# Kernel optimization log

Hardware: AMD Instinct MI355X
Metric: run time of the kernel (lower is better)

## Reference

```python
import jax, jax.numpy as jnp
import numpy as np

C = 256
NH = 4  # attention heads
G = 8   # groupnorm groups
EPS = 1e-5


def group_norm(x, weight, bias):
    B, Cc, H, W = x.shape
    xg = x.reshape(B, G, Cc // G, H, W)
    mean = xg.mean(axis=(2, 3, 4), keepdims=True)
    var = xg.var(axis=(2, 3, 4), keepdims=True)
    xg = (xg - mean) * jax.lax.rsqrt(var + EPS)
    xn = xg.reshape(B, Cc, H, W)
    return xn * weight[None, :, None, None] + bias[None, :, None, None]


def setup_inputs() -> dict:
    key = jax.random.key(0)
    ks = jax.random.split(key, 7)
    B, H, W = 16, 32, 32
    x = jax.random.normal(ks[0], (B, C, H, W), dtype=jnp.float32)
    n_weight = jnp.ones((C,), dtype=jnp.float32)
    n_bias = jnp.zeros((C,), dtype=jnp.float32)
    qkv_w = jax.random.normal(ks[1], (3 * C, C), dtype=jnp.float32) * (C ** -0.5)
    qkv_b = jnp.zeros((3 * C,), dtype=jnp.float32)
    p_w = jax.random.normal(ks[2], (C, C), dtype=jnp.float32) * (C ** -0.5)
    p_b = jnp.zeros((C,), dtype=jnp.float32)
    return {"x": x, "n_weight": n_weight, "n_bias": n_bias,
            "qkv_w": qkv_w, "qkv_b": qkv_b, "p_w": p_w, "p_b": p_b}


def reference(x, n_weight, n_bias, qkv_w, qkv_b, p_w, p_b):
    B, Cc, H, W = x.shape
    N = H * W
    dh = Cc // NH
    sc = dh ** -0.5
    xn = group_norm(x, n_weight, n_bias)  # [B,C,H,W]
    xn_flat = xn.reshape(B, Cc, N)
    # 1x1 conv == channel matmul
    qkv = jnp.einsum('oc,bcn->bon', qkv_w, xn_flat) + qkv_b[None, :, None]
    qkv = qkv.reshape(B, 3, NH, dh, N)
    q, k, v = qkv[:, 0], qkv[:, 1], qkv[:, 2]  # [B,h,dh,N]
    a = jax.nn.softmax(jnp.einsum('bhci,bhcj->bhij', q, k) * sc, axis=-1)
    o = jnp.einsum('bhij,bhcj->bhci', a, v).reshape(B, Cc, N)
    proj = jnp.einsum('oc,bcn->bon', p_w, o) + p_b[None, :, None]
    return x + proj.reshape(B, Cc, H, W)
```

## Files before the change

kernel.cpp:

```cpp
#include <hip/hip_runtime.h>
#include <math.h>

typedef unsigned short ushort;
typedef unsigned int uint;
typedef __attribute__((ext_vector_type(8))) short bf16x8;
typedef __attribute__((ext_vector_type(4))) float f32x4;
typedef __attribute__((ext_vector_type(16))) float f32x16;
typedef __attribute__((ext_vector_type(2))) unsigned uint2v;

constexpr int Bc  = 16;
constexpr float EPSc = 1e-5f;
constexpr float QSC  = 0.18033688f;

__device__ inline ushort f2bf(float f) {
    uint u = __float_as_uint(f);
    uint r = (u + 0x7fffu + ((u >> 16) & 1u)) >> 16;
    return (ushort)r;
}
__device__ __forceinline__ uint cvt2(float a, float b) {
    uint r;
    asm("v_cvt_pk_bf16_f32 %0, %1, %2" : "=v"(r) : "v"(a), "v"(b));
    return r;
}
__device__ __forceinline__ ushort f2bf_fast(float f) {
    uint r;
    asm("v_cvt_pk_bf16_f32 %0, %1, %2" : "=v"(r) : "v"(f), "v"(f));
    return (ushort)r;
}
__device__ __forceinline__ uint2v plswap(uint a, uint b) {
#if __has_builtin(__builtin_amdgcn_permlane32_swap)
    return __builtin_amdgcn_permlane32_swap(a, b, false, false);
#else
    asm volatile("v_permlane32_swap_b32 %0, %1" : "+v"(a), "+v"(b));
    uint2v r; r.x = a; r.y = b; return r;
#endif
}
#if __has_builtin(__builtin_amdgcn_exp2f)
#define EXP2F(x) __builtin_amdgcn_exp2f(x)
#else
#define EXP2F(x) __expf((x) * 0.69314718f)
#endif
__device__ __forceinline__ void gl_lds16(const ushort* g, ushort* l) {
    __builtin_amdgcn_global_load_lds(
        (const __attribute__((address_space(1))) void*)g,
        (__attribute__((address_space(3))) void*)l, 16, 0, 0);
}

__global__ __launch_bounds__(1024, 4) void norm_k(
    const float* __restrict__ x, const float* __restrict__ nw,
    const float* __restrict__ nb, const float* __restrict__ qkvw,
    const float* __restrict__ pw, ushort* __restrict__ xt,
    ushort* __restrict__ wqb, ushort* __restrict__ pwb) {
    int blk = blockIdx.x;
    int t = threadIdx.x;
    if (blk < 128) {
        int b = blk >> 3, g = blk & 7;
        const float* xs = x + ((size_t)(b * 8 + g)) * 32768;
        const float4* p4 = (const float4*)xs;
        float s = 0.f, s2 = 0.f;
#pragma unroll
        for (int i = 0; i < 8; ++i) {
            float4 v = p4[t + i * 1024];
            s += (v.x + v.y) + (v.z + v.w);
            s2 += (v.x * v.x + v.y * v.y) + (v.z * v.z + v.w * v.w);
        }
#pragma unroll
        for (int off = 1; off < 64; off <<= 1) {
            s += __shfl_xor(s, off);
            s2 += __shfl_xor(s2, off);
        }
        __shared__ float rs[16], rq[16], bc[2];
        int wv = t >> 6, lane = t & 63;
        if (lane == 0) { rs[wv] = s; rq[wv] = s2; }
        __syncthreads();
        if (t == 0) {
            float ts = 0.f, tq = 0.f;
#pragma unroll
            for (int i = 0; i < 16; ++i) { ts += rs[i]; tq += rq[i]; }
            float mean = ts * (1.f / 32768.f);
            float var  = tq * (1.f / 32768.f) - mean * mean;
            bc[0] = mean; bc[1] = rsqrtf(var + EPSc);
        }
        __syncthreads();
        float mean = bc[0], inv = bc[1];
        int n = t;
        uint w[16];
#pragma unroll
        for (int c = 0; c < 32; c += 2) {
            float w0 = inv * nw[g * 32 + c];
            float b0 = nb[g * 32 + c] - mean * w0;
            float w1 = inv * nw[g * 32 + c + 1];
            float b1 = nb[g * 32 + c + 1] - mean * w1;
            float v0 = xs[(size_t)c * 1024 + n] * w0 + b0;
            float v1 = xs[(size_t)(c + 1) * 1024 + n] * w1 + b1;
            w[c >> 1] = cvt2(v0, v1);
        }
        ushort* dst = &xt[((size_t)(b * 1024 + n)) * 256 + g * 32];
#pragma unroll
        for (int i = 0; i < 4; ++i) {
            uint4 u; u.x = w[i*4]; u.y = w[i*4+1]; u.z = w[i*4+2]; u.w = w[i*4+3];
            *(uint4*)&dst[i * 8] = u;
        }
    } else {
        int idx = ((blk - 128) * 1024 + t) * 4;
        if (idx < 196608) {
            int row = idx >> 8;
            float sc = (row < 256) ? QSC : 1.f;
            float4 v = *(const float4*)&qkvw[idx];
            uint2 u; u.x = cvt2(v.x * sc, v.y * sc); u.y = cvt2(v.z * sc, v.w * sc);
            *(uint2*)&wqb[idx] = u;
        } else {
            int j = idx - 196608;
            float4 v = *(const float4*)&pw[j];
            uint2 u; u.x = cvt2(v.x, v.y); u.y = cvt2(v.z, v.w);
            *(uint2*)&pwb[j] = u;
        }
    }
}

__global__ __launch_bounds__(256, 2) void qkv_gemm_k(
    const ushort* __restrict__ wq, const ushort* __restrict__ xt,
    const float* __restrict__ wb, ushort* __restrict__ qkT,
    ushort* __restrict__ vbuf) {
    int b = blockIdx.z, cy = blockIdx.y, sx = blockIdx.x;
    __shared__ ushort SB[2][2][128 * 64];
    int t = threadIdx.x, lane = t & 63, w = t >> 6;
    int quad = lane >> 4, l15 = lane & 15;
    int wm = w >> 1, wn = w & 1;
    const ushort* wrow = wq + (size_t)cy * 128 * 256;
    const ushort* xrow = xt + ((size_t)b * 1024 + sx * 128) * 256;
    bool tpath = (cy < 4);
    int r0 = t >> 3;
    int cs = (t & 7) ^ (r0 & 7);
    int dst = t * 8;
#pragma unroll
    for (int ps = 0; ps < 4; ++ps) {
        int r = r0 + ps * 32;
        gl_lds16(&wrow[(size_t)r * 256 + cs * 8], &SB[0][0][ps * 2048 + dst]);
        gl_lds16(&xrow[(size_t)r * 256 + cs * 8], &SB[0][1][ps * 2048 + dst]);
    }
    __syncthreads();
    int s0 = quad ^ (l15 & 7);
    f32x4 acc[4][4] = {};
    int cur = 0;
    for (int ki = 0; ki < 4; ++ki) {
        if (ki < 3) {
            int k0 = (ki + 1) * 64, nx = cur ^ 1;
#pragma unroll
            for (int ps = 0; ps < 4; ++ps) {
                int r = r0 + ps * 32;
                gl_lds16(&wrow[(size_t)r * 256 + k0 + cs * 8], &SB[nx][0][ps * 2048 + dst]);
                gl_lds16(&xrow[(size_t)r * 256 + k0 + cs * 8], &SB[nx][1][ps * 2048 + dst]);
            }
        }
        const ushort* Wc = SB[cur][0];
        const ushort* Xc = SB[cur][1];
        const ushort* Am = tpath ? Xc : Wc;
        const ushort* Bn = tpath ? Wc : Xc;
#pragma unroll
        for (int kk = 0; kk < 2; ++kk) {
            int sl = s0 ^ (kk * 4);
            bf16x8 fa[4], fb[4];
#pragma unroll
            for (int mi = 0; mi < 4; ++mi)
                fa[mi] = *(const bf16x8*)&Am[(wm * 64 + mi * 16 + l15) * 64 + sl * 8];
#pragma unroll
            for (int ni = 0; ni < 4; ++ni)
                fb[ni] = *(const bf16x8*)&Bn[(wn * 64 + ni * 16 + l15) * 64 + sl * 8];
#pragma unroll
            for (int mi = 0; mi < 4; ++mi)
#pragma unroll
                for (int ni = 0; ni < 4; ++ni)
                    acc[mi][ni] = __builtin_amdgcn_mfma_f32_16x16x32_bf16(
                        fa[mi], fb[ni], acc[mi][ni], 0, 0, 0);
        }
        __syncthreads();
        cur ^= 1;
    }
    __syncthreads();
    ushort* Tw = ((ushort*)SB) + w * (64 * 72);
    float bsc = (tpath && cy < 2) ? QSC : 1.f;
    if (tpath) {
#pragma unroll
        for (int ni = 0; ni < 4; ++ni) {
            float bias = wb[cy * 128 + wn * 64 + ni * 16 + l15] * bsc;
#pragma unroll
            for (int mi = 0; mi < 4; ++mi)
#pragma unroll
                for (int rr = 0; rr < 4; ++rr)
                    Tw[(mi * 16 + quad * 4 + rr) * 72 + ni * 16 + l15] =
                        f2bf_fast(acc[mi][ni][rr] + bias);
        }
    } else {
#pragma unroll
        for (int mi = 0; mi < 4; ++mi)
#pragma unroll
            for (int rr = 0; rr < 4; ++rr) {
                float bias = wb[cy * 128 + wm * 64 + mi * 16 + quad * 4 + rr];
#pragma unroll
                for (int ni = 0; ni < 4; ++ni)
                    Tw[(mi * 16 + quad * 4 + rr) * 72 + ni * 16 + l15] =
                        f2bf_fast(acc[mi][ni][rr] + bias);
            }
    }
    __asm__ __volatile__("" ::: "memory");
    int row8 = lane >> 3, ch = lane & 7;
#pragma unroll
    for (int p = 0; p < 8; ++p) {
        int row = p * 8 + row8;
        uint4 u = *(const uint4*)&Tw[row * 72 + ch * 8];
        if (tpath) {
            int sp = sx * 128 + wm * 64 + row;
            *(uint4*)&qkT[((size_t)b * 1024 + sp) * 512 + cy * 128 + wn * 64 + ch * 8] = u;
        } else {
            int chanloc = (cy - 4) * 128 + wm * 64 + row;
            *(uint4*)&vbuf[((size_t)b * 256 + chanloc) * 1024 + sx * 128 + wn * 64 + ch * 8] = u;
        }
    }
}

__global__ __launch_bounds__(256, 2) void attn_k(
    const ushort* __restrict__ qkT, const ushort* __restrict__ vbuf,
    ushort* __restrict__ ot) {
    int bh = blockIdx.x;
    int i0 = blockIdx.y * 128;
    int b = bh >> 2, h = bh & 3;
    const ushort* qTb = qkT + (size_t)b * 1024 * 512 + h * 64;
    const ushort* kTb = qTb + 256;
    const ushort* vb  = vbuf + ((size_t)(b * 256 + h * 64)) * 1024;
    __shared__ ushort SM[16384];
    ushort* Ks0 = SM;
    ushort* Vs0 = SM + 8192;
    int t = threadIdx.x, lane = t & 63, wv = t >> 6;
    int l31 = lane & 31, hf = lane >> 5;
    int r0 = t >> 3, pc = t & 7;
#pragma unroll
    for (int seg = 0; seg < 2; ++seg) {
        int row = seg * 32 + r0;
        int c = pc ^ (row & 7);
        gl_lds16(&kTb[(size_t)row * 512 + c * 8], &Ks0[seg * 2048 + t * 8]);
        gl_lds16(&vb[(size_t)row * 1024 + c * 8], &Vs0[seg * 2048 + t * 8]);
    }
    bf16x8 qf[4];
#pragma unroll
    for (int ks = 0; ks < 4; ++ks)
        qf[ks] = *(const bf16x8*)
            &qTb[(size_t)(i0 + wv * 32 + l31) * 512 + ks * 16 + hf * 8];
    __syncthreads();
    f32x16 oT0 = {}, oT1 = {};
    float lsum = 0.f;
    int cur = 0;
    for (int j0 = 0; j0 < 1024; j0 += 64) {
        ushort* Kc = Ks0 + cur * 4096;
        ushort* Vc = Vs0 + cur * 4096;
        if (j0 < 960) {
            int nx = cur ^ 1;
            ushort* Kn = Ks0 + nx * 4096;
            ushort* Vn = Vs0 + nx * 4096;
#pragma unroll
            for (int seg = 0; seg < 2; ++seg) {
                int row = seg * 32 + r0;
                int c = pc ^ (row & 7);
                gl_lds16(&kTb[(size_t)(j0 + 64 + row) * 512 + c * 8], &Kn[seg * 2048 + t * 8]);
                gl_lds16(&vb[(size_t)row * 1024 + j0 + 64 + c * 8],   &Vn[seg * 2048 + t * 8]);
            }
        }
#pragma unroll
        for (int jb = 0; jb < 2; ++jb) {
            f32x16 s = {};
            __builtin_amdgcn_s_setprio(1);
#pragma unroll
            for (int ks = 0; ks < 4; ++ks) {
                int row = jb * 32 + l31;
                int c = (2 * ks + hf) ^ (row & 7);
                bf16x8 ak = *(const bf16x8*)&Kc[row * 64 + c * 8];
                s = __builtin_amdgcn_mfma_f32_32x32x16_bf16(ak, qf[ks], s, 0, 0, 0);
            }
            __builtin_amdgcn_s_setprio(0);
            float e[16];
#pragma unroll
            for (int r = 0; r < 16; ++r) e[r] = EXP2F(s[r]);
            lsum += ((e[0] + e[1]) + (e[2] + e[3])) + ((e[4] + e[5]) + (e[6] + e[7]))
                  + ((e[8] + e[9]) + (e[10] + e[11])) + ((e[12] + e[13]) + (e[14] + e[15]));
            uint w0[4], w1[4];
#pragma unroll
            for (int q = 0; q < 4; ++q) {
                w0[q] = cvt2(e[q * 4 + 0], e[q * 4 + 1]);
                w1[q] = cvt2(e[q * 4 + 2], e[q * 4 + 3]);
            }
            bf16x8 pf[2];
#pragma unroll
            for (int s2 = 0; s2 < 2; ++s2) {
                uint2v ra = plswap(w0[2 * s2], w0[2 * s2 + 1]);
                uint2v rb = plswap(w1[2 * s2], w1[2 * s2 + 1]);
                uint4 u; u.x = ra.x; u.y = rb.x; u.z = ra.y; u.w = rb.y;
                bf16x8 v; __builtin_memcpy(&v, &u, 16);
                pf[s2] = v;
            }
            __builtin_amdgcn_s_setprio(1);
#pragma unroll
            for (int s2 = 0; s2 < 2; ++s2) {
#pragma unroll
                for (int db = 0; db < 2; ++db) {
                    int row = db * 32 + l31;
                    int c = (2 * (jb * 2 + s2) + hf) ^ (row & 7);
                    bf16x8 av = *(const bf16x8*)&Vc[row * 64 + c * 8];
                    if (db == 0)
                        oT0 = __builtin_amdgcn_mfma_f32_32x32x16_bf16(av, pf[s2], oT0, 0, 0, 0);
                    else
                        oT1 = __builtin_amdgcn_mfma_f32_32x32x16_bf16(av, pf[s2], oT1, 0, 0, 0);
                }
            }
            __builtin_amdgcn_s_setprio(0);
        }
        __syncthreads();
        cur ^= 1;
    }
    lsum += __shfl_xor(lsum, 32);
    float linv = 1.f / lsum;
    uint* Os = (uint*)SM + wv * (32 * 33);
#pragma unroll
    for (int db = 0; db < 2; ++db) {
        f32x16 ov = (db == 0) ? oT0 : oT1;
        int irow = l31;
#pragma unroll
        for (int q = 0; q < 4; ++q) {
            uint wa  = cvt2(ov[q * 4 + 0] * linv, ov[q * 4 + 1] * linv);
            uint wb2 = cvt2(ov[q * 4 + 2] * linv, ov[q * 4 + 3] * linv);
            int base = irow * 33 + db * 16 + q * 4 + 2 * hf;
            Os[base]     = wa;
            Os[base + 1] = wb2;
        }
    }
    __asm__ __volatile__("" ::: "memory");
#pragma unroll
    for (int rr = 0; rr < 4; ++rr) {
        int irow = (lane >> 3) + rr * 8;
        const uint* rp = &Os[irow * 33 + (lane & 7) * 4];
        uint4 u; u.x = rp[0]; u.y = rp[1]; u.z = rp[2]; u.w = rp[3];
        *(uint4*)&ot[((size_t)b * 1024 + i0 + wv * 32 + irow) * 256 + h * 64 + (lane & 7) * 8] = u;
    }
}

__global__ __launch_bounds__(256, 3) void proj_k(
    const ushort* __restrict__ pwb, const ushort* __restrict__ ot,
    const float* __restrict__ pb, const float* __restrict__ x,
    float* __restrict__ out) {
    int b = blockIdx.z, cy = blockIdx.y, sx = blockIdx.x;
    __shared__ ushort SB[2][12288];
    int t = threadIdx.x, lane = t & 63, w = t >> 6;
    int quad = lane >> 4, l15 = lane & 15;
    int wm = w >> 1, wn = w & 1;
    const ushort* wrow = pwb + (size_t)cy * 128 * 256;
    const ushort* xrow = ot + ((size_t)b * 1024 + sx * 64) * 256;
    int r0 = t >> 3;
    int cs = (t & 7) ^ (r0 & 7);
    int dst = t * 8;
#pragma unroll
    for (int ps = 0; ps < 4; ++ps)
        gl_lds16(&wrow[(size_t)(r0 + ps * 32) * 256 + cs * 8], &SB[0][ps * 2048 + dst]);
#pragma unroll
    for (int ps = 0; ps < 2; ++ps)
        gl_lds16(&xrow[(size_t)(r0 + ps * 32) * 256 + cs * 8], &SB[0][8192 + ps * 2048 + dst]);
    __syncthreads();
    int p0 = quad ^ (l15 & 7);
    f32x4 acc[4][2] = {};
    int cur = 0;
    for (int ki = 0; ki < 4; ++ki) {
        if (ki < 3) {
            int k0 = (ki + 1) * 64, nx = cur ^ 1;
#pragma unroll
            for (int ps = 0; ps < 4; ++ps)
                gl_lds16(&wrow[(size_t)(r0 + ps * 32) * 256 + k0 + cs * 8], &SB[nx][ps * 2048 + dst]);
#pragma unroll
            for (int ps = 0; ps < 2; ++ps)
                gl_lds16(&xrow[(size_t)(r0 + ps * 32) * 256 + k0 + cs * 8], &SB[nx][8192 + ps * 2048 + dst]);
        }
        const ushort* Wc = &SB[cur][0];
        const ushort* Xc = &SB[cur][8192];
#pragma unroll
        for (int kk = 0; kk < 2; ++kk) {
            int sl = p0 ^ (kk * 4);
            bf16x8 fa[4], fb[2];
#pragma unroll
            for (int mi = 0; mi < 4; ++mi)
                fa[mi] = *(const bf16x8*)&Wc[(wm * 64 + mi * 16 + l15) * 64 + sl * 8];
#pragma unroll
            for (int ni = 0; ni < 2; ++ni)
                fb[ni] = *(const bf16x8*)&Xc[(wn * 32 + ni * 16 + l15) * 64 + sl * 8];
#pragma unroll
            for (int mi = 0; mi < 4; ++mi)
#pragma unroll
                for (int ni = 0; ni < 2; ++ni)
                    acc[mi][ni] = __builtin_amdgcn_mfma_f32_16x16x32_bf16(
                        fa[mi], fb[ni], acc[mi][ni], 0, 0, 0);
        }
        __syncthreads();
        cur ^= 1;
    }
#pragma unroll
    for (int mi = 0; mi < 4; ++mi)
#pragma unroll
        for (int rr = 0; rr < 4; ++rr) {
            int chan = cy * 128 + wm * 64 + mi * 16 + quad * 4 + rr;
            float bias = pb[chan];
#pragma unroll
            for (int ni = 0; ni < 2; ++ni) {
                int sp = sx * 64 + wn * 32 + ni * 16 + l15;
                size_t o = ((size_t)(b * 256 + chan)) * 1024 + sp;
                out[o] = acc[mi][ni][rr] + bias + x[o];
            }
        }
}

extern "C" void kernel_launch(void* const* d_in, const int* in_sizes, int n_in,
                              void* d_out, int out_size, void* d_ws, size_t ws_size,
                              hipStream_t stream) {
    const float* x    = (const float*)d_in[0];
    const float* nw   = (const float*)d_in[1];
    const float* nb   = (const float*)d_in[2];
    const float* qkvw = (const float*)d_in[3];
    const float* qkvb = (const float*)d_in[4];
    const float* pw   = (const float*)d_in[5];
    const float* pb   = (const float*)d_in[6];
    float* out = (float*)d_out;

    ushort* base = (ushort*)d_ws;
    ushort* xt   = base;
    ushort* wqb  = xt + (size_t)16 * 1024 * 256;
    ushort* pwb  = wqb + 768 * 256;
    ushort* qkT  = pwb + 256 * 256;
    ushort* vbuf = qkT + (size_t)16 * 1024 * 512;
    ushort* ot   = xt;

    norm_k<<<dim3(192), dim3(1024), 0, stream>>>(x, nw, nb, qkvw, pw, xt, wqb, pwb);
    qkv_gemm_k<<<dim3(8, 6, Bc), dim3(256), 0, stream>>>(wqb, xt, qkvb, qkT, vbuf);
    attn_k<<<dim3(64, 8), dim3(256), 0, stream>>>(qkT, vbuf, ot);
    proj_k<<<dim3(16, 2, Bc), dim3(256), 0, stream>>>(pwb, ot, pb, x, out);
}
```

Baseline: 126.3 us.

## Split attention key blocks across two wave groups and cache groupnorm tile in LDS

The attention kernel now runs 512 threads, with two groups of four waves each handling one half of every 64-key tile. Partial outputs and row sums are then combined through shared memory before the normalized result is written. This raises wave-level parallelism and latency hiding per block, at the cost of an extra LDS reduction and two more barriers. Separately, the groupnorm kernel stages the whole 128KB group slice in LDS during the statistics pass, so the normalize pass reads it from LDS instead of reloading it from global memory. That cuts occupancy of that kernel to one block per CU.

```diff
diff --git a/kernel.cpp b/kernel.cpp
--- a/kernel.cpp
+++ b/kernel.cpp
@@ -12,11 +12,6 @@
 constexpr float EPSc = 1e-5f;
 constexpr float QSC  = 0.18033688f;
 
-__device__ inline ushort f2bf(float f) {
-    uint u = __float_as_uint(f);
-    uint r = (u + 0x7fffu + ((u >> 16) & 1u)) >> 16;
-    return (ushort)r;
-}
 __device__ __forceinline__ uint cvt2(float a, float b) {
     uint r;
     asm("v_cvt_pk_bf16_f32 %0, %1, %2" : "=v"(r) : "v"(a), "v"(b));
@@ -51,6 +46,8 @@
     const float* __restrict__ nb, const float* __restrict__ qkvw,
     const float* __restrict__ pw, ushort* __restrict__ xt,
     ushort* __restrict__ wqb, ushort* __restrict__ pwb) {
+    __shared__ float XS[32768];
+    __shared__ float rs[16], rq[16], bc[2];
     int blk = blockIdx.x;
     int t = threadIdx.x;
     if (blk < 128) {
@@ -63,13 +60,13 @@
             float4 v = p4[t + i * 1024];
             s += (v.x + v.y) + (v.z + v.w);
             s2 += (v.x * v.x + v.y * v.y) + (v.z * v.z + v.w * v.w);
+            *(float4*)&XS[(t + i * 1024) * 4] = v;
         }
 #pragma unroll
         for (int off = 1; off < 64; off <<= 1) {
             s += __shfl_xor(s, off);
             s2 += __shfl_xor(s2, off);
         }
-        __shared__ float rs[16], rq[16], bc[2];
         int wv = t >> 6, lane = t & 63;
         if (lane == 0) { rs[wv] = s; rq[wv] = s2; }
         __syncthreads();
@@ -91,8 +88,8 @@
             float b0 = nb[g * 32 + c] - mean * w0;
             float w1 = inv * nw[g * 32 + c + 1];
             float b1 = nb[g * 32 + c + 1] - mean * w1;
-            float v0 = xs[(size_t)c * 1024 + n] * w0 + b0;
-            float v1 = xs[(size_t)(c + 1) * 1024 + n] * w1 + b1;
+            float v0 = XS[c * 1024 + n] * w0 + b0;
+            float v1 = XS[(c + 1) * 1024 + n] * w1 + b1;
             w[c >> 1] = cvt2(v0, v1);
         }
         ushort* dst = &xt[((size_t)(b * 1024 + n)) * 256 + g * 32];
@@ -219,7 +216,7 @@
     }
 }
 
-__global__ __launch_bounds__(256, 2) void attn_k(
+__global__ __launch_bounds__(512, 4) void attn_k(
     const ushort* __restrict__ qkT, const ushort* __restrict__ vbuf,
     ushort* __restrict__ ot) {
     int bh = blockIdx.x;
@@ -229,23 +226,23 @@
     const ushort* kTb = qTb + 256;
     const ushort* vb  = vbuf + ((size_t)(b * 256 + h * 64)) * 1024;
     __shared__ ushort SM[16384];
+    __shared__ float LS[4][32];
     ushort* Ks0 = SM;
     ushort* Vs0 = SM + 8192;
     int t = threadIdx.x, lane = t & 63, wv = t >> 6;
+    int iw = wv & 3, jw = wv >> 2;
     int l31 = lane & 31, hf = lane >> 5;
-    int r0 = t >> 3, pc = t & 7;
-#pragma unroll
-    for (int seg = 0; seg < 2; ++seg) {
-        int row = seg * 32 + r0;
-        int c = pc ^ (row & 7);
-        gl_lds16(&kTb[(size_t)row * 512 + c * 8], &Ks0[seg * 2048 + t * 8]);
-        gl_lds16(&vb[(size_t)row * 1024 + c * 8], &Vs0[seg * 2048 + t * 8]);
+    int srow = t >> 3, pc = t & 7;
+    {
+        int c = pc ^ (srow & 7);
+        gl_lds16(&kTb[(size_t)srow * 512 + c * 8], &Ks0[t * 8]);
+        gl_lds16(&vb[(size_t)srow * 1024 + c * 8], &Vs0[t * 8]);
     }
     bf16x8 qf[4];
 #pragma unroll
     for (int ks = 0; ks < 4; ++ks)
         qf[ks] = *(const bf16x8*)
-            &qTb[(size_t)(i0 + wv * 32 + l31) * 512 + ks * 16 + hf * 8];
+            &qTb[(size_t)(i0 + iw * 32 + l31) * 512 + ks * 16 + hf * 8];
     __syncthreads();
     f32x16 oT0 = {}, oT1 = {};
     float lsum = 0.f;
@@ -255,90 +252,103 @@
         ushort* Vc = Vs0 + cur * 4096;
         if (j0 < 960) {
             int nx = cur ^ 1;
-            ushort* Kn = Ks0 + nx * 4096;
-            ushort* Vn = Vs0 + nx * 4096;
-#pragma unroll
-            for (int seg = 0; seg < 2; ++seg) {
-                int row = seg * 32 + r0;
-                int c = pc ^ (row & 7);
-                gl_lds16(&kTb[(size_t)(j0 + 64 + row) * 512 + c * 8], &Kn[seg * 2048 + t * 8]);
-                gl_lds16(&vb[(size_t)row * 1024 + j0 + 64 + c * 8],   &Vn[seg * 2048 + t * 8]);
+            int c = pc ^ (srow & 7);
+            gl_lds16(&kTb[(size_t)(j0 + 64 + srow) * 512 + c * 8], &Ks0[nx * 4096 + t * 8]);
+            gl_lds16(&vb[(size_t)srow * 1024 + j0 + 64 + c * 8],   &Vs0[nx * 4096 + t * 8]);
+        }
+        f32x16 s = {};
+        __builtin_amdgcn_s_setprio(1);
+#pragma unroll
+        for (int ks = 0; ks < 4; ++ks) {
+            int row = jw * 32 + l31;
+            int c = (2 * ks + hf) ^ (row & 7);
+            bf16x8 ak = *(const bf16x8*)&Kc[row * 64 + c * 8];
+            s = __builtin_amdgcn_mfma_f32_32x32x16_bf16(ak, qf[ks], s, 0, 0, 0);
+        }
+        __builtin_amdgcn_s_setprio(0);
+        uint w0[4], w1[4];
+#pragma unroll
+        for (int q = 0; q < 4; ++q) {
+            float e0 = EXP2F(s[q * 4 + 0]), e1 = EXP2F(s[q * 4 + 1]);
+            float e2 = EXP2F(s[q * 4 + 2]), e3 = EXP2F(s[q * 4 + 3]);
+            lsum += (e0 + e1) + (e2 + e3);
+            w0[q] = cvt2(e0, e1);
+            w1[q] = cvt2(e2, e3);
+        }
+        bf16x8 pf[2];
+#pragma unroll
+        for (int s2 = 0; s2 < 2; ++s2) {
+            uint2v ra = plswap(w0[2 * s2], w0[2 * s2 + 1]);
+            uint2v rb = plswap(w1[2 * s2], w1[2 * s2 + 1]);
+            uint4 u; u.x = ra.x; u.y = rb.x; u.z = ra.y; u.w = rb.y;
+            bf16x8 v; __builtin_memcpy(&v, &u, 16);
+            pf[s2] = v;
+        }
+        __builtin_amdgcn_s_setprio(1);
+#pragma unroll
+        for (int s2 = 0; s2 < 2; ++s2) {
+#pragma unroll
+            for (int db = 0; db < 2; ++db) {
+                int row = db * 32 + l31;
+                int c = (2 * (jw * 2 + s2) + hf) ^ (row & 7);
+                bf16x8 av = *(const bf16x8*)&Vc[row * 64 + c * 8];
+                if (db == 0)
+                    oT0 = __builtin_amdgcn_mfma_f32_32x32x16_bf16(av, pf[s2], oT0, 0, 0, 0);
+                else
+                    oT1 = __builtin_amdgcn_mfma_f32_32x32x16_bf16(av, pf[s2], oT1, 0, 0, 0);
             }
         }
-#pragma unroll
-        for (int jb = 0; jb < 2; ++jb) {
-            f32x16 s = {};
-            __builtin_amdgcn_s_setprio(1);
-#pragma unroll
-            for (int ks = 0; ks < 4; ++ks) {
-                int row = jb * 32 + l31;
-                int c = (2 * ks + hf) ^ (row & 7);
-                bf16x8 ak = *(const bf16x8*)&Kc[row * 64 + c * 8];
-                s = __builtin_amdgcn_mfma_f32_32x32x16_bf16(ak, qf[ks], s, 0, 0, 0);
-            }
-            __builtin_amdgcn_s_setprio(0);
-            float e[16];
-#pragma unroll
-            for (int r = 0; r < 16; ++r) e[r] = EXP2F(s[r]);
-            lsum += ((e[0] + e[1]) + (e[2] + e[3])) + ((e[4] + e[5]) + (e[6] + e[7]))
-                  + ((e[8] + e[9]) + (e[10] + e[11])) + ((e[12] + e[13]) + (e[14] + e[15]));
-            uint w0[4], w1[4];
-#pragma unroll
-            for (int q = 0; q < 4; ++q) {
-                w0[q] = cvt2(e[q * 4 + 0], e[q * 4 + 1]);
-                w1[q] = cvt2(e[q * 4 + 2], e[q * 4 + 3]);
-            }
-            bf16x8 pf[2];
-#pragma unroll
-            for (int s2 = 0; s2 < 2; ++s2) {
-                uint2v ra = plswap(w0[2 * s2], w0[2 * s2 + 1]);
-                uint2v rb = plswap(w1[2 * s2], w1[2 * s2 + 1]);
-                uint4 u; u.x = ra.x; u.y = rb.x; u.z = ra.y; u.w = rb.y;
-                bf16x8 v; __builtin_memcpy(&v, &u, 16);
-                pf[s2] = v;
-            }
-            __builtin_amdgcn_s_setprio(1);
-#pragma unroll
-            for (int s2 = 0; s2 < 2; ++s2) {
-#pragma unroll
-                for (int db = 0; db < 2; ++db) {
-                    int row = db * 32 + l31;
-                    int c = (2 * (jb * 2 + s2) + hf) ^ (row & 7);
-                    bf16x8 av = *(const bf16x8*)&Vc[row * 64 + c * 8];
-                    if (db == 0)
-                        oT0 = __builtin_amdgcn_mfma_f32_32x32x16_bf16(av, pf[s2], oT0, 0, 0, 0);
-                    else
-                        oT1 = __builtin_amdgcn_mfma_f32_32x32x16_bf16(av, pf[s2], oT1, 0, 0, 0);
-                }
-            }
-            __builtin_amdgcn_s_setprio(0);
-        }
+        __builtin_amdgcn_s_setprio(0);
         __syncthreads();
         cur ^= 1;
     }
     lsum += __shfl_xor(lsum, 32);
-    float linv = 1.f / lsum;
-    uint* Os = (uint*)SM + wv * (32 * 33);
-#pragma unroll
-    for (int db = 0; db < 2; ++db) {
-        f32x16 ov = (db == 0) ? oT0 : oT1;
-        int irow = l31;
-#pragma unroll
-        for (int q = 0; q < 4; ++q) {
-            uint wa  = cvt2(ov[q * 4 + 0] * linv, ov[q * 4 + 1] * linv);
-            uint wb2 = cvt2(ov[q * 4 + 2] * linv, ov[q * 4 + 3] * linv);
-            int base = irow * 33 + db * 16 + q * 4 + 2 * hf;
-            Os[base]     = wa;
-            Os[base + 1] = wb2;
-        }
-    }
-    __asm__ __volatile__("" ::: "memory");
-#pragma unroll
-    for (int rr = 0; rr < 4; ++rr) {
-        int irow = (lane >> 3) + rr * 8;
-        const uint* rp = &Os[irow * 33 + (lane & 7) * 4];
-        uint4 u; u.x = rp[0]; u.y = rp[1]; u.z = rp[2]; u.w = rp[3];
-        *(uint4*)&ot[((size_t)b * 1024 + i0 + wv * 32 + irow) * 256 + h * 64 + (lane & 7) * 8] = u;
+    float* OB = (float*)SM;
+    if (jw == 1) {
+        float* ob = OB + iw * 2048;
+#pragma unroll
+        for (int r = 0; r < 16; ++r) {
+            int d = (r & 3) + 8 * (r >> 2) + 4 * hf;
+            ob[d * 32 + l31]        = oT0[r];
+            ob[(d + 32) * 32 + l31] = oT1[r];
+        }
+        if (lane < 32) LS[iw][l31] = lsum;
+    }
+    __syncthreads();
+    if (jw == 0) {
+        float* ob = OB + iw * 2048;
+#pragma unroll
+        for (int r = 0; r < 16; ++r) {
+            int d = (r & 3) + 8 * (r >> 2) + 4 * hf;
+            oT0[r] += ob[d * 32 + l31];
+            oT1[r] += ob[(d + 32) * 32 + l31];
+        }
+        lsum += LS[iw][l31];
+    }
+    __syncthreads();
+    if (jw == 0) {
+        float linv = 1.f / lsum;
+        uint* Os = (uint*)SM + iw * (32 * 33);
+#pragma unroll
+        for (int db = 0; db < 2; ++db) {
+            f32x16 ov = (db == 0) ? oT0 : oT1;
+#pragma unroll
+            for (int q = 0; q < 4; ++q) {
+                uint wa  = cvt2(ov[q * 4 + 0] * linv, ov[q * 4 + 1] * linv);
+                uint wb2 = cvt2(ov[q * 4 + 2] * linv, ov[q * 4 + 3] * linv);
+                int base = l31 * 33 + db * 16 + q * 4 + 2 * hf;
+                Os[base]     = wa;
+                Os[base + 1] = wb2;
+            }
+        }
+        __asm__ __volatile__("" ::: "memory");
+#pragma unroll
+        for (int rr = 0; rr < 4; ++rr) {
+            int irow = (lane >> 3) + rr * 8;
+            const uint* rp = &Os[irow * 33 + (lane & 7) * 4];
+            uint4 u; u.x = rp[0]; u.y = rp[1]; u.z = rp[2]; u.w = rp[3];
+            *(uint4*)&ot[((size_t)b * 1024 + i0 + iw * 32 + irow) * 256 + h * 64 + (lane & 7) * 8] = u;
+        }
     }
 }
 
@@ -435,6 +445,6 @@
 
     norm_k<<<dim3(192), dim3(1024), 0, stream>>>(x, nw, nb, qkvw, pw, xt, wqb, pwb);
     qkv_gemm_k<<<dim3(8, 6, Bc), dim3(256), 0, stream>>>(wqb, xt, qkvb, qkT, vbuf);
-    attn_k<<<dim3(64, 8), dim3(256), 0, stream>>>(qkT, vbuf, ot);
+    attn_k<<<dim3(64, 8), dim3(512), 0, stream>>>(qkT, vbuf, ot);
     proj_k<<<dim3(16, 2, Bc), dim3(256), 0, stream>>>(pwb, ot, pb, x, out);
 }
```

New measurement: 130.3 us. 1.03x slower.

## Double attention KV tile to 128 keys and stage groupnorm input in LDS

Applied to the files above, without the earlier changes.

The attention kernel now loads 128 keys per pipeline stage instead of 64, so it runs half as many loop iterations and block-wide barriers. The cost is twice the LDS per block (64 KB), which may reduce how many blocks fit per CU. The groupnorm kernel now keeps the 128 KB slice of x it reads for the statistics in shared memory and normalizes from there, instead of reading global memory a second time. That much LDS allows only one block per CU, and the XS array is also allocated by the weight-conversion blocks, which never use it.

```diff
diff --git a/kernel.cpp b/kernel.cpp
--- a/kernel.cpp
+++ b/kernel.cpp
@@ -12,11 +12,6 @@
 constexpr float EPSc = 1e-5f;
 constexpr float QSC  = 0.18033688f;
 
-__device__ inline ushort f2bf(float f) {
-    uint u = __float_as_uint(f);
-    uint r = (u + 0x7fffu + ((u >> 16) & 1u)) >> 16;
-    return (ushort)r;
-}
 __device__ __forceinline__ uint cvt2(float a, float b) {
     uint r;
     asm("v_cvt_pk_bf16_f32 %0, %1, %2" : "=v"(r) : "v"(a), "v"(b));
@@ -51,6 +46,8 @@
     const float* __restrict__ nb, const float* __restrict__ qkvw,
     const float* __restrict__ pw, ushort* __restrict__ xt,
     ushort* __restrict__ wqb, ushort* __restrict__ pwb) {
+    __shared__ float XS[32768];
+    __shared__ float rs[16], rq[16], bc[2];
     int blk = blockIdx.x;
     int t = threadIdx.x;
     if (blk < 128) {
@@ -63,13 +60,13 @@
             float4 v = p4[t + i * 1024];
             s += (v.x + v.y) + (v.z + v.w);
             s2 += (v.x * v.x + v.y * v.y) + (v.z * v.z + v.w * v.w);
+            *(float4*)&XS[(t + i * 1024) * 4] = v;
         }
 #pragma unroll
         for (int off = 1; off < 64; off <<= 1) {
             s += __shfl_xor(s, off);
             s2 += __shfl_xor(s2, off);
         }
-        __shared__ float rs[16], rq[16], bc[2];
         int wv = t >> 6, lane = t & 63;
         if (lane == 0) { rs[wv] = s; rq[wv] = s2; }
         __syncthreads();
@@ -91,8 +88,8 @@
             float b0 = nb[g * 32 + c] - mean * w0;
             float w1 = inv * nw[g * 32 + c + 1];
             float b1 = nb[g * 32 + c + 1] - mean * w1;
-            float v0 = xs[(size_t)c * 1024 + n] * w0 + b0;
-            float v1 = xs[(size_t)(c + 1) * 1024 + n] * w1 + b1;
+            float v0 = XS[c * 1024 + n] * w0 + b0;
+            float v1 = XS[(c + 1) * 1024 + n] * w1 + b1;
             w[c >> 1] = cvt2(v0, v1);
         }
         ushort* dst = &xt[((size_t)(b * 1024 + n)) * 256 + g * 32];
@@ -228,18 +225,21 @@
     const ushort* qTb = qkT + (size_t)b * 1024 * 512 + h * 64;
     const ushort* kTb = qTb + 256;
     const ushort* vb  = vbuf + ((size_t)(b * 256 + h * 64)) * 1024;
-    __shared__ ushort SM[16384];
+    __shared__ ushort SM[32768];
     ushort* Ks0 = SM;
-    ushort* Vs0 = SM + 8192;
+    ushort* Vs0 = SM + 16384;
     int t = threadIdx.x, lane = t & 63, wv = t >> 6;
     int l31 = lane & 31, hf = lane >> 5;
-    int r0 = t >> 3, pc = t & 7;
-#pragma unroll
-    for (int seg = 0; seg < 2; ++seg) {
-        int row = seg * 32 + r0;
-        int c = pc ^ (row & 7);
-        gl_lds16(&kTb[(size_t)row * 512 + c * 8], &Ks0[seg * 2048 + t * 8]);
-        gl_lds16(&vb[(size_t)row * 1024 + c * 8], &Vs0[seg * 2048 + t * 8]);
+    int rk = t >> 3, pk = t & 7;
+    int rv = t >> 4, pv = t & 15;
+#pragma unroll
+    for (int seg = 0; seg < 4; ++seg) {
+        int krow = seg * 32 + rk;
+        int kc = pk ^ (krow & 7);
+        gl_lds16(&kTb[(size_t)krow * 512 + kc * 8], &Ks0[seg * 2048 + t * 8]);
+        int vrow = seg * 16 + rv;
+        int vc = pv ^ (vrow & 7);
+        gl_lds16(&vb[(size_t)vrow * 1024 + vc * 8], &Vs0[seg * 2048 + t * 8]);
     }
     bf16x8 qf[4];
 #pragma unroll
@@ -250,23 +250,25 @@
     f32x16 oT0 = {}, oT1 = {};
     float lsum = 0.f;
     int cur = 0;
-    for (int j0 = 0; j0 < 1024; j0 += 64) {
-        ushort* Kc = Ks0 + cur * 4096;
-        ushort* Vc = Vs0 + cur * 4096;
-        if (j0 < 960) {
+    for (int j0 = 0; j0 < 1024; j0 += 128) {
+        ushort* Kc = Ks0 + cur * 8192;
+        ushort* Vc = Vs0 + cur * 8192;
+        if (j0 < 896) {
             int nx = cur ^ 1;
-            ushort* Kn = Ks0 + nx * 4096;
-            ushort* Vn = Vs0 + nx * 4096;
-#pragma unroll
-            for (int seg = 0; seg < 2; ++seg) {
-                int row = seg * 32 + r0;
-                int c = pc ^ (row & 7);
-                gl_lds16(&kTb[(size_t)(j0 + 64 + row) * 512 + c * 8], &Kn[seg * 2048 + t * 8]);
-                gl_lds16(&vb[(size_t)row * 1024 + j0 + 64 + c * 8],   &Vn[seg * 2048 + t * 8]);
-            }
-        }
-#pragma unroll
-        for (int jb = 0; jb < 2; ++jb) {
+            ushort* Kn = Ks0 + nx * 8192;
+            ushort* Vn = Vs0 + nx * 8192;
+#pragma unroll
+            for (int seg = 0; seg < 4; ++seg) {
+                int krow = seg * 32 + rk;
+                int kc = pk ^ (krow & 7);
+                gl_lds16(&kTb[(size_t)(j0 + 128 + krow) * 512 + kc * 8], &Kn[seg * 2048 + t * 8]);
+                int vrow = seg * 16 + rv;
+                int vc = pv ^ (vrow & 7);
+                gl_lds16(&vb[(size_t)vrow * 1024 + j0 + 128 + vc * 8], &Vn[seg * 2048 + t * 8]);
+            }
+        }
+#pragma unroll
+        for (int jb = 0; jb < 4; ++jb) {
             f32x16 s = {};
             __builtin_amdgcn_s_setprio(1);
 #pragma unroll
@@ -277,16 +279,14 @@
                 s = __builtin_amdgcn_mfma_f32_32x32x16_bf16(ak, qf[ks], s, 0, 0, 0);
             }
             __builtin_amdgcn_s_setprio(0);
-            float e[16];
-#pragma unroll
-            for (int r = 0; r < 16; ++r) e[r] = EXP2F(s[r]);
-            lsum += ((e[0] + e[1]) + (e[2] + e[3])) + ((e[4] + e[5]) + (e[6] + e[7]))
-                  + ((e[8] + e[9]) + (e[10] + e[11])) + ((e[12] + e[13]) + (e[14] + e[15]));
             uint w0[4], w1[4];
 #pragma unroll
             for (int q = 0; q < 4; ++q) {
-                w0[q] = cvt2(e[q * 4 + 0], e[q * 4 + 1]);
-                w1[q] = cvt2(e[q * 4 + 2], e[q * 4 + 3]);
+                float e0 = EXP2F(s[q * 4 + 0]), e1 = EXP2F(s[q * 4 + 1]);
+                float e2 = EXP2F(s[q * 4 + 2]), e3 = EXP2F(s[q * 4 + 3]);
+                lsum += (e0 + e1) + (e2 + e3);
+                w0[q] = cvt2(e0, e1);
+                w1[q] = cvt2(e2, e3);
             }
             bf16x8 pf[2];
 #pragma unroll
@@ -303,8 +303,8 @@
 #pragma unroll
                 for (int db = 0; db < 2; ++db) {
                     int row = db * 32 + l31;
-                    int c = (2 * (jb * 2 + s2) + hf) ^ (row & 7);
-                    bf16x8 av = *(const bf16x8*)&Vc[row * 64 + c * 8];
+                    int c = (jb * 4 + s2 * 2 + hf) ^ (row & 7);
+                    bf16x8 av = *(const bf16x8*)&Vc[row * 128 + c * 8];
                     if (db == 0)
                         oT0 = __builtin_amdgcn_mfma_f32_32x32x16_bf16(av, pf[s2], oT0, 0, 0, 0);
                     else
@@ -322,12 +322,11 @@
 #pragma unroll
     for (int db = 0; db < 2; ++db) {
         f32x16 ov = (db == 0) ? oT0 : oT1;
-        int irow = l31;
 #pragma unroll
         for (int q = 0; q < 4; ++q) {
             uint wa  = cvt2(ov[q * 4 + 0] * linv, ov[q * 4 + 1] * linv);
             uint wb2 = cvt2(ov[q * 4 + 2] * linv, ov[q * 4 + 3] * linv);
-            int base = irow * 33 + db * 16 + q * 4 + 2 * hf;
+            int base = l31 * 33 + db * 16 + q * 4 + 2 * hf;
             Os[base]     = wa;
             Os[base + 1] = wb2;
         }
```

Result: slower. 129.3 us (+2.4%).
